# Kernel tuning notes

Hardware: AMD Instinct MI355X
Metric: run time of the kernel (lower is better)

Reference implementation:

```python
import jax, jax.numpy as jnp
import numpy as np

B, S, D = 1, 512, 3072      # batch, seq, llm_dim (Llama-3.2-3B hidden)
DH = 256                    # history_dim
E = 4                       # num_persona_experts
F = 8192                    # Llama-3.2-3B MLP intermediate size
R = 16                      # LoRA rank (alpha=16 -> scaling = 1.0)
H1 = 128                    # fusion hidden
LN_EPS = 1e-5
TOPK = 2


def setup_inputs() -> dict:
    key = jax.random.key(0)
    ks = jax.random.split(key, 24)
    sd = 0.02
    inp = {
        'x': jax.random.normal(ks[0], (B, S, D), jnp.float32),
        'history_hidden_embedding': jax.random.normal(ks[1], (B, DH), jnp.float32),
        'persona_embedding': jax.random.normal(ks[2], (E, D), jnp.float32),
        # fusion layer: Linear(2D+DH,128) split into x/history/persona blocks, ReLU, Linear(128,D), ReLU, LayerNorm(D)
        'fw1x': jax.random.normal(ks[3], (H1, D), jnp.float32) * sd,
        'fw1h': jax.random.normal(ks[4], (H1, DH), jnp.float32) * sd,
        'fw1p': jax.random.normal(ks[5], (H1, D), jnp.float32) * sd,
        'fb1': jnp.zeros((H1,), jnp.float32),
        'fw2': jax.random.normal(ks[6], (D, H1), jnp.float32) * sd,
        'fb2': jnp.zeros((D,), jnp.float32),
        'ln_g': jnp.ones((D,), jnp.float32),
        'ln_b': jnp.zeros((D,), jnp.float32),
        # scalar gate head Linear(D, 1)
        'gate_w': jax.random.normal(ks[7], (D,), jnp.float32) * sd,
        'gate_b': jnp.zeros((), jnp.float32),
        # per-expert LoRA-adapted Llama MLP (SwiGLU, no bias), stacked over E
        'Wgate': jax.random.normal(ks[8], (E, F, D), jnp.float32) * sd,
        'Wup': jax.random.normal(ks[9], (E, F, D), jnp.float32) * sd,
        'Wdown': jax.random.normal(ks[10], (E, D, F), jnp.float32) * sd,
        'Agate': jax.random.normal(ks[11], (E, R, D), jnp.float32) * sd,
        'Bgate': jax.random.normal(ks[12], (E, F, R), jnp.float32) * 0.01,
        'Aup': jax.random.normal(ks[13], (E, R, D), jnp.float32) * sd,
        'Bup': jax.random.normal(ks[14], (E, F, R), jnp.float32) * 0.01,
        'Adown': jax.random.normal(ks[15], (E, R, F), jnp.float32) * sd,
        'Bdown': jax.random.normal(ks[16], (E, D, R), jnp.float32) * 0.01,
    }
    return inp


def _layernorm(x, g, b):
    mu = jnp.mean(x, axis=-1, keepdims=True)
    var = jnp.mean(jnp.square(x - mu), axis=-1, keepdims=True)
    return (x - mu) * jax.lax.rsqrt(var + LN_EPS) * g + b


def _lora_linear(x, W, A, Bm):
    # y = x @ W^T + (x @ A^T) @ B^T  (LoRA scaling alpha/r = 1, dropout off in eval)
    base = jnp.einsum('ebsd,efd->ebsf', x, W)
    low = jnp.einsum('ebsr,efr->ebsf', jnp.einsum('ebsd,erd->ebsr', x, A), Bm)
    return base + low


def reference(x, history_hidden_embedding, persona_embedding,
              fw1x, fw1h, fw1p, fb1, fw2, fb2, ln_g, ln_b, gate_w, gate_b,
              Wgate, Wup, Wdown, Agate, Bgate, Aup, Bup, Adown, Bdown):
    # ---- gating: fusion MLP over concat(x, history, persona_e), vectorized over experts ----
    h1 = (jnp.einsum('bsd,kd->bsk', x, fw1x)
          + jnp.einsum('bh,kh->bk', history_hidden_embedding, fw1h)[:, None, :]
          + fb1)                                    # [B,S,H1]
    hp = jnp.einsum('ed,kd->ek', persona_embedding, fw1p)  # [E,H1]
    h1 = jax.nn.relu(h1[None] + hp[:, None, None, :])      # [E,B,S,H1]
    fused = jax.nn.relu(jnp.einsum('ebsk,dk->ebsd', h1, fw2) + fb2)
    fused = _layernorm(fused, ln_g, ln_b)                  # [E,B,S,D]
    logits = jnp.einsum('ebsd,d->ebs', fused, gate_w) + gate_b
    logits = jnp.moveaxis(logits, 0, -1)                   # [B,S,E]
    gate_probs = jax.nn.softmax(logits, axis=-1)
    # ---- top-k=2 selection; combine weights are raw probs at selected slots ----
    _, top_i = jax.lax.top_k(gate_probs, TOPK)
    sel = jax.nn.one_hot(top_i, gate_probs.shape[-1], dtype=gate_probs.dtype).sum(-2)  # [B,S,E]
    w = gate_probs * sel
    # ---- experts: LoRA SwiGLU FFN, dense-equivalent combine (unselected weight = 0) ----
    xe = jnp.broadcast_to(x[None], (Wgate.shape[0],) + x.shape)  # [E,B,S,D]
    g = _lora_linear(xe, Wgate, Agate, Bgate)
    u = _lora_linear(xe, Wup, Aup, Bup)
    h = jax.nn.silu(g) * u                                       # [E,B,S,F]
    d = (jnp.einsum('ebsf,edf->ebsd', h, Wdown)
         + jnp.einsum('ebsr,edr->ebsd', jnp.einsum('ebsf,erf->ebsr', h, Adown), Bdown))
    out = jnp.einsum('ebsd,bse->bsd', d, w)                      # weighted scatter-add combine
    entropy = -(gate_probs * jnp.log(gate_probs + 1e-9)).sum(-1).mean()
    return out, entropy
```

## Files before the change

### kernel.cpp

```cpp
#include <hip/hip_runtime.h>

#define TS 512
#define TD 3072
#define TDH 256
#define TE 4
#define TF 8192
#define TR 16
#define TH1 128

typedef unsigned short u16;
typedef unsigned int u32;

typedef short short8 __attribute__((ext_vector_type(8)));
typedef float f32x4 __attribute__((ext_vector_type(4)));

__device__ __forceinline__ u16 f2bf(float f) {
  union { float f; u32 u; } v; v.f = f;
  u32 r = v.u + 0x7fffu + ((v.u >> 16) & 1u);
  return (u16)(r >> 16);
}
__device__ __forceinline__ u32 pk2(float a, float b) {
  return (u32)f2bf(a) | ((u32)f2bf(b) << 16);
}
__device__ __forceinline__ float bflo(u32 v) {
  union { u32 u; float f; } w; w.u = v << 16; return w.f;
}
__device__ __forceinline__ float bfhi(u32 v) {
  union { u32 u; float f; } w; w.u = v & 0xffff0000u; return w.f;
}
__device__ __forceinline__ float wred(float v) {
  #pragma unroll
  for (int o = 32; o; o >>= 1) v += __shfl_down(v, o);
  return v;
}
__device__ __forceinline__ float dot4(float4 a, float4 b) {
  return a.x*b.x + a.y*b.y + a.z*b.z + a.w*b.w;
}

__global__ void k_zero(float* __restrict__ p, int n) {
  for (int i = blockIdx.x * blockDim.x + threadIdx.x; i < n; i += gridDim.x * blockDim.x)
    p[i] = 0.f;
}

__global__ void k_prep(const float* __restrict__ hist, const float* __restrict__ fw1h,
                       const float* __restrict__ fb1, const float* __restrict__ persona,
                       const float* __restrict__ fw1p, const float* __restrict__ lng,
                       const float* __restrict__ lnb, const float* __restrict__ gw,
                       float* __restrict__ hb, float* __restrict__ hp, float* __restrict__ sc)
{
  const int k = blockIdx.x, t = threadIdx.x;
  if (k < TH1) {
    float a = 0.f;
    for (int h = t; h < TDH; h += 64) a += hist[h] * fw1h[k * TDH + h];
    a = wred(a);
    if (t == 0) hb[k] = a + fb1[k];
    for (int e = 0; e < TE; ++e) {
      float b = 0.f;
      for (int d = t; d < TD; d += 64) b += persona[e * TD + d] * fw1p[k * TD + d];
      b = wred(b);
      if (t == 0) hp[e * TH1 + k] = b;
    }
  } else {
    float g = 0.f, bb = 0.f;
    for (int d = t; d < TD; d += 64) { g += lng[d] * gw[d]; bb += lnb[d] * gw[d]; }
    g = wred(g); bb = wred(bb);
    if (t == 0) { sc[0] = g; sc[1] = bb; }
  }
}

__global__ void k_h1(const float* __restrict__ x, const float* __restrict__ fw1x,
                     const float* __restrict__ hb, float* __restrict__ h1)
{
  const int s0 = blockIdx.x * 4, t = threadIdx.x;
  __shared__ float xr[4][TD];
  for (int r = 0; r < 4; ++r)
    for (int i = t; i < TD / 4; i += 128)
      ((float4*)xr[r])[i] = ((const float4*)(x + (size_t)(s0 + r) * TD))[i];
  __syncthreads();
  float a0 = 0.f, a1 = 0.f, a2 = 0.f, a3 = 0.f;
  const float4* wp = (const float4*)(fw1x + (size_t)t * TD);
  for (int c = 0; c < TD / 4; ++c) {
    float4 wv = wp[c];
    a0 += dot4(wv, ((const float4*)xr[0])[c]);
    a1 += dot4(wv, ((const float4*)xr[1])[c]);
    a2 += dot4(wv, ((const float4*)xr[2])[c]);
    a3 += dot4(wv, ((const float4*)xr[3])[c]);
  }
  const float hv = hb[t];
  h1[(s0 + 0) * TH1 + t] = a0 + hv;
  h1[(s0 + 1) * TH1 + t] = a1 + hv;
  h1[(s0 + 2) * TH1 + t] = a2 + hv;
  h1[(s0 + 3) * TH1 + t] = a3 + hv;
}

__global__ void k_logits(const float* __restrict__ h1, const float* __restrict__ hp,
                         const float* __restrict__ fw2, const float* __restrict__ fb2,
                         const float* __restrict__ lng, const float* __restrict__ lnb,
                         const float* __restrict__ gw, const float* __restrict__ gbp,
                         const float* __restrict__ sc, float* __restrict__ logits)
{
  const int s = blockIdx.x, t = threadIdx.x;
  __shared__ float h1e[TE][TH1];
  __shared__ float red[4][12];
  if (t < TH1) {
    const float base = h1[s * TH1 + t];
    #pragma unroll
    for (int e = 0; e < TE; ++e) {
      float v = base + hp[e * TH1 + t];
      h1e[e][t] = v > 0.f ? v : 0.f;
    }
  }
  __syncthreads();
  float acc[12][4];
  #pragma unroll
  for (int dd = 0; dd < 12; ++dd)
    #pragma unroll
    for (int e = 0; e < 4; ++e) acc[dd][e] = 0.f;

  for (int c = 0; c < 32; ++c) {
    float4 h4[TE];
    #pragma unroll
    for (int e = 0; e < TE; ++e) h4[e] = *(const float4*)&h1e[e][c * 4];
    #pragma unroll
    for (int dd = 0; dd < 12; ++dd) {
      const int d = t + dd * 256;
      float4 wv = *(const float4*)(fw2 + (size_t)d * TH1 + c * 4);
      #pragma unroll
      for (int e = 0; e < TE; ++e) acc[dd][e] += dot4(wv, h4[e]);
    }
  }
  float s1[4] = {0,0,0,0}, s2[4] = {0,0,0,0}, s3[4] = {0,0,0,0};
  #pragma unroll
  for (int dd = 0; dd < 12; ++dd) {
    const int d = t + dd * 256;
    const float fb = fb2[d];
    const float ggw = lng[d] * gw[d];
    #pragma unroll
    for (int e = 0; e < 4; ++e) {
      float f = acc[dd][e] + fb;
      f = fmaxf(f, 0.f);
      s1[e] += f; s2[e] += f * f; s3[e] += f * ggw;
    }
  }
  #pragma unroll
  for (int e = 0; e < 4; ++e) { s1[e] = wred(s1[e]); s2[e] = wred(s2[e]); s3[e] = wred(s3[e]); }
  const int lane = t & 63, w = t >> 6;
  if (lane == 0) {
    #pragma unroll
    for (int e = 0; e < 4; ++e) { red[w][e] = s1[e]; red[w][4 + e] = s2[e]; red[w][8 + e] = s3[e]; }
  }
  __syncthreads();
  if (t == 0) {
    const float dotg = sc[0], dotb = sc[1], gb = gbp[0];
    #pragma unroll
    for (int e = 0; e < 4; ++e) {
      float S1 = red[0][e] + red[1][e] + red[2][e] + red[3][e];
      float S2 = red[0][4+e] + red[1][4+e] + red[2][4+e] + red[3][4+e];
      float S3 = red[0][8+e] + red[1][8+e] + red[2][8+e] + red[3][8+e];
      float mu = S1 * (1.f / TD);
      float var = S2 * (1.f / TD) - mu * mu;
      float rs = 1.f / sqrtf(var + 1e-5f);
      logits[e * TS + s] = rs * (S3 - mu * dotg) + dotb + gb;
    }
  }
}

__global__ void k_gate(const float* __restrict__ logits, float* __restrict__ wbuf,
                       float* __restrict__ entOut)
{
  const int s = threadIdx.x;
  float l[4], p[4];
  #pragma unroll
  for (int e = 0; e < 4; ++e) l[e] = logits[e * TS + s];
  float m = fmaxf(fmaxf(l[0], l[1]), fmaxf(l[2], l[3]));
  float sum = 0.f;
  #pragma unroll
  for (int e = 0; e < 4; ++e) { p[e] = expf(l[e] - m); sum += p[e]; }
  const float inv = 1.f / sum;
  #pragma unroll
  for (int e = 0; e < 4; ++e) p[e] *= inv;
  int i1 = 0; float b1 = p[0];
  #pragma unroll
  for (int e = 1; e < 4; ++e) if (p[e] > b1) { b1 = p[e]; i1 = e; }
  int i2 = -1; float b2 = -1.f;
  #pragma unroll
  for (int e = 0; e < 4; ++e) if (e != i1 && p[e] > b2) { b2 = p[e]; i2 = e; }
  float ent = 0.f;
  #pragma unroll
  for (int e = 0; e < 4; ++e) {
    ent -= p[e] * logf(p[e] + 1e-9f);
    wbuf[s * TE + e] = (e == i1 || e == i2) ? p[e] : 0.f;
  }
  ent = wred(ent);
  __shared__ float red[8];
  if ((s & 63) == 0) red[s >> 6] = ent;
  __syncthreads();
  if (s == 0) {
    float tot = 0.f;
    #pragma unroll
    for (int w = 0; w < 8; ++w) tot += red[w];
    entOut[0] = tot * (1.f / TS);
  }
}

__global__ void k_cvtx(const float* __restrict__ x, u16* __restrict__ xbf) {
  const size_t i = ((size_t)blockIdx.x * 256 + threadIdx.x) * 4;
  float4 v = *(const float4*)(x + i);
  uint2 o; o.x = pk2(v.x, v.y); o.y = pk2(v.z, v.w);
  *(uint2*)(xbf + i) = o;
}

__global__ void k_xa(const float* __restrict__ x, const float* __restrict__ Ag,
                     const float* __restrict__ Au, u16* __restrict__ xag, u16* __restrict__ xau)
{
  const int e = blockIdx.x, s = blockIdx.y, t = threadIdx.x;
  const int wavei = t >> 6, lane = t & 63;
  const int r = lane & 15, q = lane >> 4;
  const float* A = wavei ? Au : Ag;
  u16* dst = wavei ? xau : xag;
  const float4* xv = (const float4*)(x + (size_t)s * TD);
  const float4* av = (const float4*)(A + ((size_t)e * TR + r) * TD);
  float acc = 0.f;
  for (int c = q * 192; c < q * 192 + 192; ++c) acc += dot4(av[c], xv[c]);
  acc += __shfl_xor(acc, 16);
  acc += __shfl_xor(acc, 32);
  if (q == 0) dst[((size_t)e * TS + s) * TR + r] = f2bf(acc);
}

__global__ __launch_bounds__(256, 2) void k_gateup(
    const float* __restrict__ Wg, const float* __restrict__ Wu,
    const float* __restrict__ Bg, const float* __restrict__ Bu,
    const u16* __restrict__ xbf, const u16* __restrict__ xag,
    const u16* __restrict__ xau, u16* __restrict__ hbuf)
{
  __shared__ __attribute__((aligned(16))) u16 lA[128 * 40];
  __shared__ __attribute__((aligned(16))) u16 lBg[128 * 40];
  __shared__ __attribute__((aligned(16))) u16 lBu[128 * 40];
  __shared__ __attribute__((aligned(16))) u16 lA2[128 * 40];
  const int e = blockIdx.z;
  const int n0 = blockIdx.x * 128;
  const int m0 = blockIdx.y * 128;
  const int t = threadIdx.x;
  const int lane = t & 63, wv = t >> 6;
  const int wm = wv >> 1, wn = wv & 1;
  const int lr = lane & 15, lk = lane >> 4;

  f32x4 accg[4][4], accu[4][4];
  #pragma unroll
  for (int i = 0; i < 4; ++i)
    #pragma unroll
    for (int j = 0; j < 4; ++j) {
      f32x4 z = {0.f, 0.f, 0.f, 0.f};
      accg[i][j] = z; accu[i][j] = z;
    }

  const int r0 = t >> 2;
  const int cc0 = (t & 3) * 8;
  const u16* Abase = xbf + (size_t)m0 * TD;
  const float* Gbase = Wg + ((size_t)e * TF + n0) * TD;
  const float* Ubase = Wu + ((size_t)e * TF + n0) * TD;

  for (int kt = 0; kt < TD; kt += 32) {
    #pragma unroll
    for (int h = 0; h < 2; ++h) {
      const int row = r0 + h * 64;
      *(uint4*)&lA[row * 40 + cc0] = *(const uint4*)(Abase + (size_t)row * TD + kt + cc0);
      const float4* gp = (const float4*)(Gbase + (size_t)row * TD + kt + cc0);
      float4 g0 = gp[0], g1 = gp[1];
      uint4 gpk; gpk.x = pk2(g0.x, g0.y); gpk.y = pk2(g0.z, g0.w);
      gpk.z = pk2(g1.x, g1.y); gpk.w = pk2(g1.z, g1.w);
      *(uint4*)&lBg[row * 40 + cc0] = gpk;
      const float4* up = (const float4*)(Ubase + (size_t)row * TD + kt + cc0);
      float4 u0 = up[0], u1 = up[1];
      uint4 upk; upk.x = pk2(u0.x, u0.y); upk.y = pk2(u0.z, u0.w);
      upk.z = pk2(u1.x, u1.y); upk.w = pk2(u1.z, u1.w);
      *(uint4*)&lBu[row * 40 + cc0] = upk;
    }
    __syncthreads();
    short8 af[4], bgf[4], buf[4];
    #pragma unroll
    for (int i = 0; i < 4; ++i) {
      af[i]  = *(const short8*)&lA [(wm * 64 + i * 16 + lr) * 40 + lk * 8];
      bgf[i] = *(const short8*)&lBg[(wn * 64 + i * 16 + lr) * 40 + lk * 8];
      buf[i] = *(const short8*)&lBu[(wn * 64 + i * 16 + lr) * 40 + lk * 8];
    }
    #pragma unroll
    for (int mi = 0; mi < 4; ++mi)
      #pragma unroll
      for (int ni = 0; ni < 4; ++ni) {
        accg[mi][ni] = __builtin_amdgcn_mfma_f32_16x16x32_bf16(af[mi], bgf[ni], accg[mi][ni], 0, 0, 0);
        accu[mi][ni] = __builtin_amdgcn_mfma_f32_16x16x32_bf16(af[mi], buf[ni], accu[mi][ni], 0, 0, 0);
      }
    __syncthreads();
  }

  for (int i = t; i < 4096; i += 256) {
    const int row = i >> 5, c = i & 31;
    u16 vag = 0, vau = 0, vbg = 0, vbu = 0;
    if (c < TR) {
      vag = xag[((size_t)e * TS + m0 + row) * TR + c];
      vau = xau[((size_t)e * TS + m0 + row) * TR + c];
      vbg = f2bf(Bg[((size_t)e * TF + n0 + row) * TR + c]);
      vbu = f2bf(Bu[((size_t)e * TF + n0 + row) * TR + c]);
    }
    lA [row * 40 + c] = vag;
    lA2[row * 40 + c] = vau;
    lBg[row * 40 + c] = vbg;
    lBu[row * 40 + c] = vbu;
  }
  __syncthreads();
  {
    short8 ag[4], au[4], bgf[4], buf[4];
    #pragma unroll
    for (int i = 0; i < 4; ++i) {
      ag[i]  = *(const short8*)&lA [(wm * 64 + i * 16 + lr) * 40 + lk * 8];
      au[i]  = *(const short8*)&lA2[(wm * 64 + i * 16 + lr) * 40 + lk * 8];
      bgf[i] = *(const short8*)&lBg[(wn * 64 + i * 16 + lr) * 40 + lk * 8];
      buf[i] = *(const short8*)&lBu[(wn * 64 + i * 16 + lr) * 40 + lk * 8];
    }
    #pragma unroll
    for (int mi = 0; mi < 4; ++mi)
      #pragma unroll
      for (int ni = 0; ni < 4; ++ni) {
        accg[mi][ni] = __builtin_amdgcn_mfma_f32_16x16x32_bf16(ag[mi], bgf[ni], accg[mi][ni], 0, 0, 0);
        accu[mi][ni] = __builtin_amdgcn_mfma_f32_16x16x32_bf16(au[mi], buf[ni], accu[mi][ni], 0, 0, 0);
      }
  }

  u16* hrow = hbuf + ((size_t)e * TS + m0) * TF + n0;
  #pragma unroll
  for (int mi = 0; mi < 4; ++mi)
    #pragma unroll
    for (int j = 0; j < 4; ++j) {
      const int srow = wm * 64 + mi * 16 + lk * 4 + j;
      #pragma unroll
      for (int ni = 0; ni < 4; ++ni) {
        const int fcol = wn * 64 + ni * 16 + lr;
        float g = accg[mi][ni][j];
        float u = accu[mi][ni][j];
        float hval = (g / (1.f + __expf(-g))) * u;
        hrow[(size_t)srow * TF + fcol] = f2bf(hval);
      }
    }
}

__global__ void k_ha(const u16* __restrict__ hbuf, const float* __restrict__ Ad,
                     u16* __restrict__ ha)
{
  const int e = blockIdx.x, s = blockIdx.y, t = threadIdx.x;
  const int wv = t >> 6, lane = t & 63;
  const int r = lane & 15, seg = (lane >> 4) + (wv << 2);
  const u16* hrow = hbuf + ((size_t)e * TS + s) * TF + seg * 512;
  const float* arow = Ad + ((size_t)e * TR + r) * TF + seg * 512;
  float acc = 0.f;
  for (int i = 0; i < 512; i += 4) {
    uint2 hv = *(const uint2*)(hrow + i);
    float4 av = *(const float4*)(arow + i);
    acc += bflo(hv.x) * av.x + bfhi(hv.x) * av.y + bflo(hv.y) * av.z + bfhi(hv.y) * av.w;
  }
  acc += __shfl_xor(acc, 16);
  acc += __shfl_xor(acc, 32);
  __shared__ float red[4][16];
  if ((lane >> 4) == 0) red[wv][r] = acc;
  __syncthreads();
  if (wv == 0 && lane < 16) {
    float tot = red[0][lane] + red[1][lane] + red[2][lane] + red[3][lane];
    ha[((size_t)e * TS + s) * TR + lane] = f2bf(tot);
  }
}

__global__ __launch_bounds__(256, 3) void k_down(
    const float* __restrict__ Wd, const float* __restrict__ Bd,
    const u16* __restrict__ hbuf, const u16* __restrict__ ha,
    const float* __restrict__ wbuf, float* __restrict__ out)
{
  __shared__ __attribute__((aligned(16))) u16 lA[128 * 40];
  __shared__ __attribute__((aligned(16))) u16 lB[128 * 40];
  const int e = blockIdx.z;
  const int n0 = blockIdx.x * 128;
  const int m0 = (blockIdx.y >> 1) * 128;
  const int kh = blockIdx.y & 1;
  const int t = threadIdx.x;
  const int lane = t & 63, wv = t >> 6;
  const int wm = wv >> 1, wn = wv & 1;
  const int lr = lane & 15, lk = lane >> 4;

  f32x4 acc[4][4];
  #pragma unroll
  for (int i = 0; i < 4; ++i)
    #pragma unroll
    for (int j = 0; j < 4; ++j) { f32x4 z = {0.f, 0.f, 0.f, 0.f}; acc[i][j] = z; }

  const int r0 = t >> 2;
  const int cc0 = (t & 3) * 8;
  const u16* Abase = hbuf + ((size_t)e * TS + m0) * TF;
  const float* Bbase = Wd + ((size_t)e * TD + n0) * TF;

  const int k0 = kh * 4096;
  for (int kt = k0; kt < k0 + 4096; kt += 32) {
    #pragma unroll
    for (int h = 0; h < 2; ++h) {
      const int row = r0 + h * 64;
      *(uint4*)&lA[row * 40 + cc0] = *(const uint4*)(Abase + (size_t)row * TF + kt + cc0);
      const float4* p = (const float4*)(Bbase + (size_t)row * TF + kt + cc0);
      float4 v0 = p[0], v1 = p[1];
      uint4 pk; pk.x = pk2(v0.x, v0.y); pk.y = pk2(v0.z, v0.w);
      pk.z = pk2(v1.x, v1.y); pk.w = pk2(v1.z, v1.w);
      *(uint4*)&lB[row * 40 + cc0] = pk;
    }
    __syncthreads();
    short8 af[4], bf[4];
    #pragma unroll
    for (int i = 0; i < 4; ++i) {
      af[i] = *(const short8*)&lA[(wm * 64 + i * 16 + lr) * 40 + lk * 8];
      bf[i] = *(const short8*)&lB[(wn * 64 + i * 16 + lr) * 40 + lk * 8];
    }
    #pragma unroll
    for (int mi = 0; mi < 4; ++mi)
      #pragma unroll
      for (int ni = 0; ni < 4; ++ni)
        acc[mi][ni] = __builtin_amdgcn_mfma_f32_16x16x32_bf16(af[mi], bf[ni], acc[mi][ni], 0, 0, 0);
    __syncthreads();
  }

  if (kh == 0) {
    for (int i = t; i < 4096; i += 256) {
      const int row = i >> 5, c = i & 31;
      u16 av = 0, bv = 0;
      if (c < TR) {
        av = ha[((size_t)e * TS + m0 + row) * TR + c];
        bv = f2bf(Bd[((size_t)e * TD + n0 + row) * TR + c]);
      }
      lA[row * 40 + c] = av;
      lB[row * 40 + c] = bv;
    }
    __syncthreads();
    short8 af[4], bf[4];
    #pragma unroll
    for (int i = 0; i < 4; ++i) {
      af[i] = *(const short8*)&lA[(wm * 64 + i * 16 + lr) * 40 + lk * 8];
      bf[i] = *(const short8*)&lB[(wn * 64 + i * 16 + lr) * 40 + lk * 8];
    }
    #pragma unroll
    for (int mi = 0; mi < 4; ++mi)
      #pragma unroll
      for (int ni = 0; ni < 4; ++ni)
        acc[mi][ni] = __builtin_amdgcn_mfma_f32_16x16x32_bf16(af[mi], bf[ni], acc[mi][ni], 0, 0, 0);
  }

  #pragma unroll
  for (int mi = 0; mi < 4; ++mi)
    #pragma unroll
    for (int j = 0; j < 4; ++j) {
      const int srow = m0 + wm * 64 + mi * 16 + lk * 4 + j;
      const float wgt = wbuf[srow * TE + e];
      if (wgt != 0.f) {
        #pragma unroll
        for (int ni = 0; ni < 4; ++ni) {
          const int dcol = n0 + wn * 64 + ni * 16 + lr;
          unsafeAtomicAdd(&out[(size_t)srow * TD + dcol], wgt * acc[mi][ni][j]);
        }
      }
    }
}

extern "C" void kernel_launch(void* const* d_in, const int* in_sizes, int n_in,
                              void* d_out, int out_size, void* d_ws, size_t ws_size,
                              hipStream_t stream) {
  const float* x       = (const float*)d_in[0];
  const float* hist    = (const float*)d_in[1];
  const float* persona = (const float*)d_in[2];
  const float* fw1x    = (const float*)d_in[3];
  const float* fw1h    = (const float*)d_in[4];
  const float* fw1p    = (const float*)d_in[5];
  const float* fb1     = (const float*)d_in[6];
  const float* fw2     = (const float*)d_in[7];
  const float* fb2     = (const float*)d_in[8];
  const float* lng     = (const float*)d_in[9];
  const float* lnb     = (const float*)d_in[10];
  const float* gw      = (const float*)d_in[11];
  const float* gb      = (const float*)d_in[12];
  const float* Wg      = (const float*)d_in[13];
  const float* Wu      = (const float*)d_in[14];
  const float* Wd      = (const float*)d_in[15];
  const float* Ag      = (const float*)d_in[16];
  const float* Bg      = (const float*)d_in[17];
  const float* Au      = (const float*)d_in[18];
  const float* Bu      = (const float*)d_in[19];
  const float* Ad      = (const float*)d_in[20];
  const float* Bd      = (const float*)d_in[21];
  float* out = (float*)d_out;

  char* wsb = (char*)d_ws;
  float* hb     = (float*)(wsb + 0);
  float* hp     = (float*)(wsb + 1024);
  float* sc     = (float*)(wsb + 3072);
  float* logits = (float*)(wsb + 4096);
  float* wbuf   = (float*)(wsb + 12288);
  float* h1     = (float*)(wsb + 20480);
  u16*   xbf    = (u16*)(wsb + 282624);
  u16*   xag    = (u16*)(wsb + 3428352);
  u16*   xau    = (u16*)(wsb + 3493888);
  u16*   habf   = (u16*)(wsb + 3559424);
  u16*   hbuf   = (u16*)(wsb + 3624960);

  k_zero<<<1024, 256, 0, stream>>>(out, out_size);
  k_prep<<<TH1 + 1, 64, 0, stream>>>(hist, fw1h, fb1, persona, fw1p, lng, lnb, gw, hb, hp, sc);
  k_h1<<<TS / 4, 128, 0, stream>>>(x, fw1x, hb, h1);
  k_logits<<<TS, 256, 0, stream>>>(h1, hp, fw2, fb2, lng, lnb, gw, gb, sc, logits);
  k_gate<<<1, TS, 0, stream>>>(logits, wbuf, out + (size_t)TS * TD);
  k_cvtx<<<(TS * TD) / 1024, 256, 0, stream>>>(x, xbf);
  k_xa<<<dim3(TE, TS), 128, 0, stream>>>(x, Ag, Au, xag, xau);
  k_gateup<<<dim3(TF / 128, TS / 128, TE), 256, 0, stream>>>(Wg, Wu, Bg, Bu, xbf, xag, xau, hbuf);
  k_ha<<<dim3(TE, TS), 256, 0, stream>>>(hbuf, Ad, habf);
  k_down<<<dim3(TD / 128, (TS / 128) * 2, TE), 256, 0, stream>>>(Wd, Bd, hbuf, habf, wbuf, out);
}
```

Measured before the change: 2.113 ms.

## Route only top-2 selected tokens per expert through gate/up and down GEMMs

The gate kernel now builds per-expert token lists and weights with shared atomics. The gate/up and down GEMMs gather only the selected token rows, and blocks beyond each expert's count exit early. With top-2 of 4 experts this roughly halves the dense expert FLOPs. It also adds register prefetch of the next K tile, a cheaper perm-based bf16 packing, and a 4-way K split in the down GEMM. Token order within each list is nondeterministic, and gathered loads are less contiguous.

```diff
diff --git a/kernel.cpp b/kernel.cpp
--- a/kernel.cpp
+++ b/kernel.cpp
@@ -14,13 +14,16 @@
 typedef short short8 __attribute__((ext_vector_type(8)));
 typedef float f32x4 __attribute__((ext_vector_type(4)));
 
+__device__ __forceinline__ int imin(int a, int b) { return a < b ? a : b; }
+
 __device__ __forceinline__ u16 f2bf(float f) {
   union { float f; u32 u; } v; v.f = f;
   u32 r = v.u + 0x7fffu + ((v.u >> 16) & 1u);
   return (u16)(r >> 16);
 }
-__device__ __forceinline__ u32 pk2(float a, float b) {
-  return (u32)f2bf(a) | ((u32)f2bf(b) << 16);
+__device__ __forceinline__ u32 pk2r(float a, float b) {
+  union { float f; u32 u; } x, y; x.f = a; y.f = b;
+  return __builtin_amdgcn_perm(y.u + 0x8000u, x.u + 0x8000u, 0x07060302u);
 }
 __device__ __forceinline__ float bflo(u32 v) {
   union { u32 u; float f; } w; w.u = v << 16; return w.f;
@@ -126,7 +129,7 @@
       const int d = t + dd * 256;
       float4 wv = *(const float4*)(fw2 + (size_t)d * TH1 + c * 4);
       #pragma unroll
-      for (int e = 0; e < TE; ++e) acc[dd][e] += dot4(wv, h4[e]);
+      for (int e = 0; e < 4; ++e) acc[dd][e] += dot4(wv, h4[e]);
     }
   }
   float s1[4] = {0,0,0,0}, s2[4] = {0,0,0,0}, s3[4] = {0,0,0,0};
@@ -165,10 +168,14 @@
   }
 }
 
-__global__ void k_gate(const float* __restrict__ logits, float* __restrict__ wbuf,
-                       float* __restrict__ entOut)
+__global__ void k_gate(const float* __restrict__ logits, float* __restrict__ entOut,
+                       int* __restrict__ cntg, int* __restrict__ toklist,
+                       float* __restrict__ wsel)
 {
   const int s = threadIdx.x;
+  __shared__ int cnt[TE];
+  if (s < TE) cnt[s] = 0;
+  __syncthreads();
   float l[4], p[4];
   #pragma unroll
   for (int e = 0; e < 4; ++e) l[e] = logits[e * TS + s];
@@ -185,12 +192,13 @@
   int i2 = -1; float b2 = -1.f;
   #pragma unroll
   for (int e = 0; e < 4; ++e) if (e != i1 && p[e] > b2) { b2 = p[e]; i2 = e; }
+  int p1 = atomicAdd(&cnt[i1], 1);
+  int p2 = atomicAdd(&cnt[i2], 1);
+  toklist[i1 * TS + p1] = s; wsel[i1 * TS + p1] = p[i1];
+  toklist[i2 * TS + p2] = s; wsel[i2 * TS + p2] = p[i2];
   float ent = 0.f;
   #pragma unroll
-  for (int e = 0; e < 4; ++e) {
-    ent -= p[e] * logf(p[e] + 1e-9f);
-    wbuf[s * TE + e] = (e == i1 || e == i2) ? p[e] : 0.f;
-  }
+  for (int e = 0; e < 4; ++e) ent -= p[e] * logf(p[e] + 1e-9f);
   ent = wred(ent);
   __shared__ float red[8];
   if ((s & 63) == 0) red[s >> 6] = ent;
@@ -201,12 +209,14 @@
     for (int w = 0; w < 8; ++w) tot += red[w];
     entOut[0] = tot * (1.f / TS);
   }
+  if (s < TE) cntg[s] = cnt[s];
 }
 
 __global__ void k_cvtx(const float* __restrict__ x, u16* __restrict__ xbf) {
   const size_t i = ((size_t)blockIdx.x * 256 + threadIdx.x) * 4;
   float4 v = *(const float4*)(x + i);
-  uint2 o; o.x = pk2(v.x, v.y); o.y = pk2(v.z, v.w);
+  uint2 o; o.x = (u32)f2bf(v.x) | ((u32)f2bf(v.y) << 16);
+  o.y = (u32)f2bf(v.z) | ((u32)f2bf(v.w) << 16);
   *(uint2*)(xbf + i) = o;
 }
 
@@ -231,19 +241,24 @@
     const float* __restrict__ Wg, const float* __restrict__ Wu,
     const float* __restrict__ Bg, const float* __restrict__ Bu,
     const u16* __restrict__ xbf, const u16* __restrict__ xag,
-    const u16* __restrict__ xau, u16* __restrict__ hbuf)
+    const u16* __restrict__ xau, const int* __restrict__ cntg,
+    const int* __restrict__ toklist, u16* __restrict__ hbuf)
 {
   __shared__ __attribute__((aligned(16))) u16 lA[128 * 40];
   __shared__ __attribute__((aligned(16))) u16 lBg[128 * 40];
   __shared__ __attribute__((aligned(16))) u16 lBu[128 * 40];
   __shared__ __attribute__((aligned(16))) u16 lA2[128 * 40];
   const int e = blockIdx.z;
+  const int cnt = cntg[e];
+  const int m0 = blockIdx.y * 128;
+  if (m0 >= cnt) return;
   const int n0 = blockIdx.x * 128;
-  const int m0 = blockIdx.y * 128;
   const int t = threadIdx.x;
   const int lane = t & 63, wv = t >> 6;
   const int wm = wv >> 1, wn = wv & 1;
   const int lr = lane & 15, lk = lane >> 4;
+  const int r0 = t >> 2;
+  const int cc0 = (t & 3) * 8;
 
   f32x4 accg[4][4], accu[4][4];
   #pragma unroll
@@ -254,29 +269,47 @@
       accg[i][j] = z; accu[i][j] = z;
     }
 
-  const int r0 = t >> 2;
-  const int cc0 = (t & 3) * 8;
-  const u16* Abase = xbf + (size_t)m0 * TD;
-  const float* Gbase = Wg + ((size_t)e * TF + n0) * TD;
-  const float* Ubase = Wu + ((size_t)e * TF + n0) * TD;
+  const int tk0 = toklist[e * TS + imin(m0 + r0, cnt - 1)];
+  const int tk1 = toklist[e * TS + imin(m0 + r0 + 64, cnt - 1)];
+  const u16* a0p = xbf + (size_t)tk0 * TD + cc0;
+  const u16* a1p = xbf + (size_t)tk1 * TD + cc0;
+  const float* g0p = Wg + ((size_t)e * TF + n0 + r0) * TD + cc0;
+  const float* g1p = g0p + (size_t)64 * TD;
+  const float* u0p = Wu + ((size_t)e * TF + n0 + r0) * TD + cc0;
+  const float* u1p = u0p + (size_t)64 * TD;
+
+  uint4 ra0 = *(const uint4*)a0p;
+  uint4 ra1 = *(const uint4*)a1p;
+  float4 rg0a = *(const float4*)g0p, rg0b = *(const float4*)(g0p + 4);
+  float4 rg1a = *(const float4*)g1p, rg1b = *(const float4*)(g1p + 4);
+  float4 ru0a = *(const float4*)u0p, ru0b = *(const float4*)(u0p + 4);
+  float4 ru1a = *(const float4*)u1p, ru1b = *(const float4*)(u1p + 4);
 
   for (int kt = 0; kt < TD; kt += 32) {
-    #pragma unroll
-    for (int h = 0; h < 2; ++h) {
-      const int row = r0 + h * 64;
-      *(uint4*)&lA[row * 40 + cc0] = *(const uint4*)(Abase + (size_t)row * TD + kt + cc0);
-      const float4* gp = (const float4*)(Gbase + (size_t)row * TD + kt + cc0);
-      float4 g0 = gp[0], g1 = gp[1];
-      uint4 gpk; gpk.x = pk2(g0.x, g0.y); gpk.y = pk2(g0.z, g0.w);
-      gpk.z = pk2(g1.x, g1.y); gpk.w = pk2(g1.z, g1.w);
-      *(uint4*)&lBg[row * 40 + cc0] = gpk;
-      const float4* up = (const float4*)(Ubase + (size_t)row * TD + kt + cc0);
-      float4 u0 = up[0], u1 = up[1];
-      uint4 upk; upk.x = pk2(u0.x, u0.y); upk.y = pk2(u0.z, u0.w);
-      upk.z = pk2(u1.x, u1.y); upk.w = pk2(u1.z, u1.w);
-      *(uint4*)&lBu[row * 40 + cc0] = upk;
-    }
+    *(uint4*)&lA[r0 * 40 + cc0] = ra0;
+    *(uint4*)&lA[(r0 + 64) * 40 + cc0] = ra1;
+    uint4 pg0, pg1, pu0, pu1;
+    pg0.x = pk2r(rg0a.x, rg0a.y); pg0.y = pk2r(rg0a.z, rg0a.w);
+    pg0.z = pk2r(rg0b.x, rg0b.y); pg0.w = pk2r(rg0b.z, rg0b.w);
+    pg1.x = pk2r(rg1a.x, rg1a.y); pg1.y = pk2r(rg1a.z, rg1a.w);
+    pg1.z = pk2r(rg1b.x, rg1b.y); pg1.w = pk2r(rg1b.z, rg1b.w);
+    pu0.x = pk2r(ru0a.x, ru0a.y); pu0.y = pk2r(ru0a.z, ru0a.w);
+    pu0.z = pk2r(ru0b.x, ru0b.y); pu0.w = pk2r(ru0b.z, ru0b.w);
+    pu1.x = pk2r(ru1a.x, ru1a.y); pu1.y = pk2r(ru1a.z, ru1a.w);
+    pu1.z = pk2r(ru1b.x, ru1b.y); pu1.w = pk2r(ru1b.z, ru1b.w);
+    *(uint4*)&lBg[r0 * 40 + cc0] = pg0;
+    *(uint4*)&lBg[(r0 + 64) * 40 + cc0] = pg1;
+    *(uint4*)&lBu[r0 * 40 + cc0] = pu0;
+    *(uint4*)&lBu[(r0 + 64) * 40 + cc0] = pu1;
     __syncthreads();
+    if (kt + 32 < TD) {
+      ra0 = *(const uint4*)(a0p + kt + 32);
+      ra1 = *(const uint4*)(a1p + kt + 32);
+      rg0a = *(const float4*)(g0p + kt + 32); rg0b = *(const float4*)(g0p + kt + 36);
+      rg1a = *(const float4*)(g1p + kt + 32); rg1b = *(const float4*)(g1p + kt + 36);
+      ru0a = *(const float4*)(u0p + kt + 32); ru0b = *(const float4*)(u0p + kt + 36);
+      ru1a = *(const float4*)(u1p + kt + 32); ru1b = *(const float4*)(u1p + kt + 36);
+    }
     short8 af[4], bgf[4], buf[4];
     #pragma unroll
     for (int i = 0; i < 4; ++i) {
@@ -298,8 +331,9 @@
     const int row = i >> 5, c = i & 31;
     u16 vag = 0, vau = 0, vbg = 0, vbu = 0;
     if (c < TR) {
-      vag = xag[((size_t)e * TS + m0 + row) * TR + c];
-      vau = xau[((size_t)e * TS + m0 + row) * TR + c];
+      const int tkr = toklist[e * TS + imin(m0 + row, cnt - 1)];
+      vag = xag[((size_t)e * TS + tkr) * TR + c];
+      vau = xau[((size_t)e * TS + tkr) * TR + c];
       vbg = f2bf(Bg[((size_t)e * TF + n0 + row) * TR + c]);
       vbu = f2bf(Bu[((size_t)e * TF + n0 + row) * TR + c]);
     }
@@ -345,17 +379,18 @@
 }
 
 __global__ void k_ha(const u16* __restrict__ hbuf, const float* __restrict__ Ad,
-                     u16* __restrict__ ha)
-{
-  const int e = blockIdx.x, s = blockIdx.y, t = threadIdx.x;
+                     const int* __restrict__ cntg, u16* __restrict__ ha)
+{
+  const int e = blockIdx.x, i = blockIdx.y, t = threadIdx.x;
+  if (i >= cntg[e]) return;
   const int wv = t >> 6, lane = t & 63;
   const int r = lane & 15, seg = (lane >> 4) + (wv << 2);
-  const u16* hrow = hbuf + ((size_t)e * TS + s) * TF + seg * 512;
+  const u16* hrow = hbuf + ((size_t)e * TS + i) * TF + seg * 512;
   const float* arow = Ad + ((size_t)e * TR + r) * TF + seg * 512;
   float acc = 0.f;
-  for (int i = 0; i < 512; i += 4) {
-    uint2 hv = *(const uint2*)(hrow + i);
-    float4 av = *(const float4*)(arow + i);
+  for (int c = 0; c < 512; c += 4) {
+    uint2 hv = *(const uint2*)(hrow + c);
+    float4 av = *(const float4*)(arow + c);
     acc += bflo(hv.x) * av.x + bfhi(hv.x) * av.y + bflo(hv.y) * av.z + bfhi(hv.y) * av.w;
   }
   acc += __shfl_xor(acc, 16);
@@ -365,25 +400,29 @@
   __syncthreads();
   if (wv == 0 && lane < 16) {
     float tot = red[0][lane] + red[1][lane] + red[2][lane] + red[3][lane];
-    ha[((size_t)e * TS + s) * TR + lane] = f2bf(tot);
-  }
-}
-
-__global__ __launch_bounds__(256, 3) void k_down(
+    ha[((size_t)e * TS + i) * TR + lane] = f2bf(tot);
+  }
+}
+
+__global__ __launch_bounds__(256, 2) void k_down(
     const float* __restrict__ Wd, const float* __restrict__ Bd,
     const u16* __restrict__ hbuf, const u16* __restrict__ ha,
-    const float* __restrict__ wbuf, float* __restrict__ out)
+    const int* __restrict__ cntg, const int* __restrict__ toklist,
+    const float* __restrict__ wsel, float* __restrict__ out)
 {
   __shared__ __attribute__((aligned(16))) u16 lA[128 * 40];
   __shared__ __attribute__((aligned(16))) u16 lB[128 * 40];
   const int e = blockIdx.z;
+  const int cnt = cntg[e];
+  const int m0 = (blockIdx.y >> 2) * 128;
+  if (m0 >= cnt) return;
+  const int kh = blockIdx.y & 3;
   const int n0 = blockIdx.x * 128;
-  const int m0 = (blockIdx.y >> 1) * 128;
-  const int kh = blockIdx.y & 1;
   const int t = threadIdx.x;
   const int lane = t & 63, wv = t >> 6;
   const int wm = wv >> 1, wn = wv & 1;
   const int lr = lane & 15, lk = lane >> 4;
+  const int r0 = t >> 2, cc0 = (t & 3) * 8;
 
   f32x4 acc[4][4];
   #pragma unroll
@@ -391,24 +430,36 @@
     #pragma unroll
     for (int j = 0; j < 4; ++j) { f32x4 z = {0.f, 0.f, 0.f, 0.f}; acc[i][j] = z; }
 
-  const int r0 = t >> 2;
-  const int cc0 = (t & 3) * 8;
-  const u16* Abase = hbuf + ((size_t)e * TS + m0) * TF;
-  const float* Bbase = Wd + ((size_t)e * TD + n0) * TF;
-
-  const int k0 = kh * 4096;
-  for (int kt = k0; kt < k0 + 4096; kt += 32) {
-    #pragma unroll
-    for (int h = 0; h < 2; ++h) {
-      const int row = r0 + h * 64;
-      *(uint4*)&lA[row * 40 + cc0] = *(const uint4*)(Abase + (size_t)row * TF + kt + cc0);
-      const float4* p = (const float4*)(Bbase + (size_t)row * TF + kt + cc0);
-      float4 v0 = p[0], v1 = p[1];
-      uint4 pk; pk.x = pk2(v0.x, v0.y); pk.y = pk2(v0.z, v0.w);
-      pk.z = pk2(v1.x, v1.y); pk.w = pk2(v1.z, v1.w);
-      *(uint4*)&lB[row * 40 + cc0] = pk;
-    }
+  const int iA0 = imin(m0 + r0, cnt - 1);
+  const int iA1 = imin(m0 + r0 + 64, cnt - 1);
+  const u16* a0p = hbuf + ((size_t)e * TS + iA0) * TF + cc0;
+  const u16* a1p = hbuf + ((size_t)e * TS + iA1) * TF + cc0;
+  const float* w0p = Wd + ((size_t)e * TD + n0 + r0) * TF + cc0;
+  const float* w1p = w0p + (size_t)64 * TF;
+
+  const int k0 = kh * 2048;
+  uint4 ra0 = *(const uint4*)(a0p + k0);
+  uint4 ra1 = *(const uint4*)(a1p + k0);
+  float4 rw0a = *(const float4*)(w0p + k0), rw0b = *(const float4*)(w0p + k0 + 4);
+  float4 rw1a = *(const float4*)(w1p + k0), rw1b = *(const float4*)(w1p + k0 + 4);
+
+  for (int kt = k0; kt < k0 + 2048; kt += 32) {
+    *(uint4*)&lA[r0 * 40 + cc0] = ra0;
+    *(uint4*)&lA[(r0 + 64) * 40 + cc0] = ra1;
+    uint4 p0, p1;
+    p0.x = pk2r(rw0a.x, rw0a.y); p0.y = pk2r(rw0a.z, rw0a.w);
+    p0.z = pk2r(rw0b.x, rw0b.y); p0.w = pk2r(rw0b.z, rw0b.w);
+    p1.x = pk2r(rw1a.x, rw1a.y); p1.y = pk2r(rw1a.z, rw1a.w);
+    p1.z = pk2r(rw1b.x, rw1b.y); p1.w = pk2r(rw1b.z, rw1b.w);
+    *(uint4*)&lB[r0 * 40 + cc0] = p0;
+    *(uint4*)&lB[(r0 + 64) * 40 + cc0] = p1;
     __syncthreads();
+    if (kt + 32 < k0 + 2048) {
+      ra0 = *(const uint4*)(a0p + kt + 32);
+      ra1 = *(const uint4*)(a1p + kt + 32);
+      rw0a = *(const float4*)(w0p + kt + 32); rw0b = *(const float4*)(w0p + kt + 36);
+      rw1a = *(const float4*)(w1p + kt + 32); rw1b = *(const float4*)(w1p + kt + 36);
+    }
     short8 af[4], bf[4];
     #pragma unroll
     for (int i = 0; i < 4; ++i) {
@@ -428,7 +479,8 @@
       const int row = i >> 5, c = i & 31;
       u16 av = 0, bv = 0;
       if (c < TR) {
-        av = ha[((size_t)e * TS + m0 + row) * TR + c];
+        const int ii = imin(m0 + row, cnt - 1);
+        av = ha[((size_t)e * TS + ii) * TR + c];
         bv = f2bf(Bd[((size_t)e * TD + n0 + row) * TR + c]);
       }
       lA[row * 40 + c] = av;
@@ -452,13 +504,15 @@
   for (int mi = 0; mi < 4; ++mi)
     #pragma unroll
     for (int j = 0; j < 4; ++j) {
-      const int srow = m0 + wm * 64 + mi * 16 + lk * 4 + j;
-      const float wgt = wbuf[srow * TE + e];
-      if (wgt != 0.f) {
+      const int srow = wm * 64 + mi * 16 + lk * 4 + j;
+      const int ip = m0 + srow;
+      if (ip < cnt) {
+        const int tok = toklist[e * TS + ip];
+        const float wgt = wsel[e * TS + ip];
         #pragma unroll
         for (int ni = 0; ni < 4; ++ni) {
           const int dcol = n0 + wn * 64 + ni * 16 + lr;
-          unsafeAtomicAdd(&out[(size_t)srow * TD + dcol], wgt * acc[mi][ni][j]);
+          unsafeAtomicAdd(&out[(size_t)tok * TD + dcol], wgt * acc[mi][ni][j]);
         }
       }
     }
@@ -492,26 +546,28 @@
   float* out = (float*)d_out;
 
   char* wsb = (char*)d_ws;
-  float* hb     = (float*)(wsb + 0);
-  float* hp     = (float*)(wsb + 1024);
-  float* sc     = (float*)(wsb + 3072);
-  float* logits = (float*)(wsb + 4096);
-  float* wbuf   = (float*)(wsb + 12288);
-  float* h1     = (float*)(wsb + 20480);
-  u16*   xbf    = (u16*)(wsb + 282624);
-  u16*   xag    = (u16*)(wsb + 3428352);
-  u16*   xau    = (u16*)(wsb + 3493888);
-  u16*   habf   = (u16*)(wsb + 3559424);
-  u16*   hbuf   = (u16*)(wsb + 3624960);
+  float* hb      = (float*)(wsb + 0);
+  float* hp      = (float*)(wsb + 1024);
+  float* sc      = (float*)(wsb + 3072);
+  float* logits  = (float*)(wsb + 4096);
+  int*   cntg    = (int*)  (wsb + 12288);
+  int*   toklist = (int*)  (wsb + 16384);
+  float* wsel    = (float*)(wsb + 24576);
+  float* h1      = (float*)(wsb + 32768);
+  u16*   xbf     = (u16*)  (wsb + 294912);
+  u16*   xag     = (u16*)  (wsb + 3440640);
+  u16*   xau     = (u16*)  (wsb + 3506176);
+  u16*   habf    = (u16*)  (wsb + 3571712);
+  u16*   hbuf    = (u16*)  (wsb + 3637248);
 
   k_zero<<<1024, 256, 0, stream>>>(out, out_size);
   k_prep<<<TH1 + 1, 64, 0, stream>>>(hist, fw1h, fb1, persona, fw1p, lng, lnb, gw, hb, hp, sc);
   k_h1<<<TS / 4, 128, 0, stream>>>(x, fw1x, hb, h1);
   k_logits<<<TS, 256, 0, stream>>>(h1, hp, fw2, fb2, lng, lnb, gw, gb, sc, logits);
-  k_gate<<<1, TS, 0, stream>>>(logits, wbuf, out + (size_t)TS * TD);
+  k_gate<<<1, TS, 0, stream>>>(logits, out + (size_t)TS * TD, cntg, toklist, wsel);
   k_cvtx<<<(TS * TD) / 1024, 256, 0, stream>>>(x, xbf);
   k_xa<<<dim3(TE, TS), 128, 0, stream>>>(x, Ag, Au, xag, xau);
-  k_gateup<<<dim3(TF / 128, TS / 128, TE), 256, 0, stream>>>(Wg, Wu, Bg, Bu, xbf, xag, xau, hbuf);
-  k_ha<<<dim3(TE, TS), 256, 0, stream>>>(hbuf, Ad, habf);
-  k_down<<<dim3(TD / 128, (TS / 128) * 2, TE), 256, 0, stream>>>(Wd, Bd, hbuf, habf, wbuf, out);
-}
+  k_gateup<<<dim3(TF / 128, TS / 128, TE), 256, 0, stream>>>(Wg, Wu, Bg, Bu, xbf, xag, xau, cntg, toklist, hbuf);
+  k_ha<<<dim3(TE, TS), 256, 0, stream>>>(hbuf, Ad, cntg, habf);
+  k_down<<<dim3(TD / 128, 16, TE), 256, 0, stream>>>(Wd, Bd, hbuf, habf, cntg, toklist, wsel, out);
+}
```

Result: faster. 1.965 ms (-7.0%).
